# Kernel optimization log

Measured on AMD Instinct MI355X. Metric: run time of the kernel, lower is better.

Reference implementation:

```python
import jax, jax.numpy as jnp
import numpy as np

N, E, B = 50000, 400000, 8
ND, ED, H, L = 32, 16, 128, 3

def setup_inputs() -> dict:
    key = jax.random.key(0)
    ks = jax.random.split(key, 32)
    s = 0.05
    inp = {
        'x': jax.random.normal(ks[0], (N, ND), jnp.float32),
        'edge_attr': jax.random.normal(ks[1], (E, ED), jnp.float32),
        'global_feature': jax.random.normal(ks[2], (B, 1), jnp.float32),
        'edge_index': jax.random.randint(ks[3], (2, E), 0, N, jnp.int64),
        'batch': jnp.sort(jax.random.randint(ks[4], (N,), 0, B, jnp.int64)),
        # embeddings
        'Wn': jax.random.normal(ks[5], (ND, H), jnp.float32) * s,
        'bn': jnp.zeros((H,), jnp.float32),
        'We': jax.random.normal(ks[6], (ED, H), jnp.float32) * s,
        'be': jnp.zeros((H,), jnp.float32),
        'Wg': jax.random.normal(ks[7], (1, H), jnp.float32) * s,
        'bg': jnp.zeros((H,), jnp.float32),
        # message-passing layers (stacked over L)
        'mW1': jax.random.normal(ks[8], (L, 3 * H, H), jnp.float32) * s,
        'mb1': jnp.zeros((L, H), jnp.float32),
        'mW2': jax.random.normal(ks[9], (L, H, H), jnp.float32) * s,
        'mb2': jnp.zeros((L, H), jnp.float32),
        'uW1': jax.random.normal(ks[10], (L, 2 * H, H), jnp.float32) * s,
        'ub1': jnp.zeros((L, H), jnp.float32),
        'uW2': jax.random.normal(ks[11], (L, H, H), jnp.float32) * s,
        'ub2': jnp.zeros((L, H), jnp.float32),
        # readout MLP
        'rW1': jax.random.normal(ks[12], (2 * H, H), jnp.float32) * s,
        'rb1': jnp.zeros((H,), jnp.float32),
        'rW2': jax.random.normal(ks[13], (H, H // 2), jnp.float32) * s,
        'rb2': jnp.zeros((H // 2,), jnp.float32),
        'rW3': jax.random.normal(ks[14], (H // 2, 1), jnp.float32) * s,
        'rb3': jnp.zeros((1,), jnp.float32),
    }
    return inp

def reference(x, edge_attr, global_feature, Wn, bn, We, be, Wg, bg,
              mW1, mb1, mW2, mb2, uW1, ub1, uW2, ub2,
              rW1, rb1, rW2, rb2, rW3, rb3, edge_index, batch):
    h = x @ Wn + bn                      # [N,H]
    e = edge_attr @ We + be              # [E,H]
    g = global_feature @ Wg + bg         # [B,H]
    src, dst = edge_index[0], edge_index[1]  # PyG: x_j=source, x_i=target, aggregate at target
    for l in range(L):
        m_in = jnp.concatenate([h[dst], h[src], e], axis=1)            # [E,3H]
        m = jax.nn.relu(m_in @ mW1[l] + mb1[l]) @ mW2[l] + mb2[l]       # [E,H]
        aggr = jax.ops.segment_sum(m, dst, num_segments=N)              # [N,H]
        u_in = jnp.concatenate([h, aggr], axis=1)                       # [N,2H]
        upd = jax.nn.relu(u_in @ uW1[l] + ub1[l]) @ uW2[l] + ub2[l]
        h = h + upd
    counts = jax.ops.segment_sum(jnp.ones((N,), h.dtype), batch, num_segments=B)
    pooled = jax.ops.segment_sum(h, batch, num_segments=B) / jnp.maximum(counts, 1.0)[:, None]
    final = jnp.concatenate([pooled, g], axis=1)                        # [B,2H]
    out = jax.nn.relu(final @ rW1 + rb1)
    out = jax.nn.relu(out @ rW2 + rb2)
    return out @ rW3 + rb3                                              # [B,1]
```

## Files before the change

kernel.cpp:

```cpp
#include <hip/hip_runtime.h>

#define NN 50000
#define NPAD 50048
#define NBLK 391
#define NE 400000
#define NBATCH 8
#define NDIM 32
#define EDIM 16
#define H 128
#define NLAYERS 3
#define CHUNK_ELEMS 4096
#define NODE_CHUNKS 24
#define ZW_CHUNK 8192
#define NSB 196
#define ZEB 128

typedef __attribute__((ext_vector_type(8))) __bf16 bf16x8;
typedef __attribute__((ext_vector_type(16))) float f32x16;
typedef __attribute__((ext_vector_type(8))) short short8;
typedef __attribute__((ext_vector_type(2))) float v2f;

__device__ __forceinline__ void block_sync_lds() {
  asm volatile("s_waitcnt lgkmcnt(0)\ns_barrier" ::: "memory");
}
__device__ __forceinline__ void wait_lds() {
  asm volatile("s_waitcnt lgkmcnt(0)" ::: "memory");
}
__device__ __forceinline__ v2f bf2f(unsigned u) {
  v2f r;
  r.x = __uint_as_float(u << 16);
  r.y = __uint_as_float(u & 0xffff0000u);
  return r;
}

__global__ __launch_bounds__(128) void embed_nodes_kernel(
    const float* __restrict__ x, const float* __restrict__ Wn,
    const float* __restrict__ bn, __bf16* __restrict__ hb) {
  __shared__ float Ws[NDIM * H];
  __shared__ float xs[16 * NDIM];
  int j = threadIdx.x;
  int nbase = blockIdx.x * 16;
  for (int r = 0; r < NDIM; ++r) Ws[r * H + j] = Wn[r * H + j];
#pragma unroll
  for (int t = 0; t < 4; ++t) {
    int f = j + t * 128;
    xs[f] = x[nbase * NDIM + f];
  }
  __syncthreads();
  float b = bn[j];
  for (int nn = 0; nn < 16; ++nn) {
    float acc = b;
#pragma unroll
    for (int k = 0; k < NDIM; ++k)
      acc = fmaf(xs[nn * NDIM + k], Ws[k * H + j], acc);
    hb[(size_t)(nbase + nn) * H + j] = (__bf16)acc;
  }
}

__global__ __launch_bounds__(256) void degree_kernel(const int* __restrict__ ei,
                                                     int* __restrict__ deg) {
  int e = blockIdx.x * 256 + threadIdx.x;
  if (e < NE) atomicAdd(&deg[ei[NE + e]], 1);
}

__global__ __launch_bounds__(256) void scan1_kernel(const int* __restrict__ deg,
                                                    int* __restrict__ bsum) {
  __shared__ int ws[4];
  int i = blockIdx.x * 256 + threadIdx.x;
  int lane = threadIdx.x & 63, wid = threadIdx.x >> 6;
  int v = (i < NN) ? deg[i] : 0;
#pragma unroll
  for (int off = 32; off; off >>= 1) v += __shfl_down(v, off);
  if (lane == 0) ws[wid] = v;
  __syncthreads();
  if (threadIdx.x == 0) bsum[blockIdx.x] = ws[0] + ws[1] + ws[2] + ws[3];
}

__global__ __launch_bounds__(256) void scan2_kernel(const int* __restrict__ bsum,
                                                    int* __restrict__ boff) {
  __shared__ int s[256];
  int t = threadIdx.x;
  int v = (t < NSB) ? bsum[t] : 0;
  s[t] = v;
  __syncthreads();
  for (int off = 1; off < 256; off <<= 1) {
    int u = (t >= off) ? s[t - off] : 0;
    __syncthreads();
    s[t] += u;
    __syncthreads();
  }
  if (t < NSB) boff[t] = s[t] - v;
}

__global__ __launch_bounds__(256) void scan3_kernel(const int* __restrict__ deg,
                                                    const int* __restrict__ boff,
                                                    int* __restrict__ cursor) {
  __shared__ int wsum[4], woff[4];
  int i = blockIdx.x * 256 + threadIdx.x;
  int lane = threadIdx.x & 63, wid = threadIdx.x >> 6;
  int orig = (i < NN) ? deg[i] : 0;
  int v = orig;
#pragma unroll
  for (int off = 1; off < 64; off <<= 1) {
    int u = __shfl_up(v, off);
    if (lane >= off) v += u;
  }
  if (lane == 63) wsum[wid] = v;
  __syncthreads();
  if (threadIdx.x == 0) {
    int r = 0;
#pragma unroll
    for (int w = 0; w < 4; ++w) {
      woff[w] = r;
      r += wsum[w];
    }
  }
  __syncthreads();
  if (i < NN) cursor[i] = (v - orig) + woff[wid] + boff[blockIdx.x];
}

__global__ __launch_bounds__(256) void scatter_kernel(
    const int* __restrict__ ei, int* __restrict__ cursor,
    int* __restrict__ srcSrt, int* __restrict__ eidSrt) {
  int e = blockIdx.x * 256 + threadIdx.x;
  if (e < NE) {
    int d = ei[NE + e];
    int pos = atomicAdd(&cursor[d], 1);
    srcSrt[pos] = ei[e];
    eidSrt[pos] = e;
  }
}

__global__ __launch_bounds__(256) void gather_ea_kernel(
    const float* __restrict__ ea, const int* __restrict__ eidSrt,
    __bf16* __restrict__ eaSrt) {
  int fl = blockIdx.x * 256 + threadIdx.x;
  if (fl < NE) {
    int e = eidSrt[fl];
    const float4* ep = (const float4*)(ea + (size_t)e * EDIM);
    __bf16* op = eaSrt + (size_t)fl * EDIM;
#pragma unroll
    for (int q = 0; q < 4; ++q) {
      float4 v = ep[q];
      op[q * 4 + 0] = (__bf16)v.x;
      op[q * 4 + 1] = (__bf16)v.y;
      op[q * 4 + 2] = (__bf16)v.z;
      op[q * 4 + 3] = (__bf16)v.w;
    }
  }
}

__global__ __launch_bounds__(256) void precomp_zw_kernel(
    const float* __restrict__ mW1, __bf16* __restrict__ ZW) {
  int l = blockIdx.x / 8;
  int c = blockIdx.x % 8;
  int tid = threadIdx.x;
  const float* w1 = mW1 + (size_t)l * 384 * H;
  __bf16* dst = ZW + ((size_t)l * 8 + c) * ZW_CHUNK;
  for (int it = 0; it < 32; ++it) {
    int flat = it * 256 + tid;
    int j = flat & 7;
    int lane = (flat >> 3) & 63;
    int nt = (flat >> 9) & 7;
    int hilo = flat >> 12;
    int k = c * 16 + ((lane >> 5) << 3) + j;
    int n = nt * 32 + (lane & 31);
    float w = (n < 128) ? w1[(size_t)k * H + n]
                        : w1[(size_t)(128 + k) * H + (n - 128)];
    __bf16 hi = (__bf16)w;
    __bf16 lo = (__bf16)(w - (float)hi);
    dst[flat] = hilo ? lo : hi;
  }
}

__global__ __launch_bounds__(128) void precomp_wef_kernel(
    const float* __restrict__ mW1, const float* __restrict__ mb1,
    const float* __restrict__ We, const float* __restrict__ be,
    float* __restrict__ Wef, float* __restrict__ bm) {
  int l = blockIdx.x;
  int n = threadIdx.x;
  const float* w1 = mW1 + (size_t)l * 384 * H;
  float acc[EDIM];
#pragma unroll
  for (int i = 0; i < EDIM; ++i) acc[i] = 0.f;
  float accb = 0.f;
  for (int c = 0; c < H; ++c) {
    float wv = w1[(size_t)(256 + c) * H + n];
    accb = fmaf(be[c], wv, accb);
#pragma unroll
    for (int i = 0; i < EDIM; ++i)
      acc[i] = fmaf(We[i * H + c], wv, acc[i]);
  }
#pragma unroll
  for (int i = 0; i < EDIM; ++i)
    Wef[((size_t)l * EDIM + i) * H + n] = acc[i];
  bm[l * H + n] = mb1[l * H + n] + accb;
}

__global__ __launch_bounds__(256) void precomp_wefs_kernel(
    const float* __restrict__ Wef, __bf16* __restrict__ WefS) {
  int l = blockIdx.x;
  int tid = threadIdx.x;
  int nt = tid >> 6, lane = tid & 63;
  int n = nt * 32 + (lane & 31);
  int half = lane >> 5;
  const float* wl = Wef + (size_t)l * EDIM * H;
  __bf16* dst = WefS + (size_t)l * CHUNK_ELEMS;
#pragma unroll
  for (int j = 0; j < 8; ++j) {
    int k = half * 8 + j;
    float w = wl[(size_t)k * H + n];
    __bf16 hi = (__bf16)w;
    __bf16 lo = (__bf16)(w - (float)hi);
    dst[((0 * 4 + nt) * 64 + lane) * 8 + j] = hi;
    dst[((1 * 4 + nt) * 64 + lane) * 8 + j] = lo;
  }
}

__global__ __launch_bounds__(128) void precomp_wu_kernel(
    const float* __restrict__ uW1, const float* __restrict__ mW2,
    const float* __restrict__ mb2, float* __restrict__ Wu,
    float* __restrict__ va) {
  int l = blockIdx.x / 257;
  int r = blockIdx.x % 257;
  int j = threadIdx.x;
  const float* u1 = uW1 + (size_t)l * 256 * H;
  if (r < 128) {
    Wu[((size_t)l * 256 + r) * H + j] = u1[(size_t)r * H + j];
  } else if (r < 256) {
    int i = r - 128;
    const float* m2 = mW2 + ((size_t)l * H + i) * H;
    float s = 0.f;
    for (int c = 0; c < H; ++c)
      s = fmaf(m2[c], u1[(size_t)(128 + c) * H + j], s);
    Wu[((size_t)l * 256 + r) * H + j] = s;
  } else {
    float s = 0.f;
    for (int c = 0; c < H; ++c)
      s = fmaf(mb2[l * H + c], u1[(size_t)(128 + c) * H + j], s);
    va[l * H + j] = s;
  }
}

__global__ __launch_bounds__(256) void precomp_wns_kernel(
    const float* __restrict__ Wu, const float* __restrict__ uW2,
    __bf16* __restrict__ WnS) {
  int l = blockIdx.x / NODE_CHUNKS;
  int c = blockIdx.x % NODE_CHUNKS;
  int tid = threadIdx.x;
  int nt = tid >> 6, lane = tid & 63;
  int n = nt * 32 + (lane & 31);
  int half = lane >> 5;
  __bf16* dst = WnS + ((size_t)l * NODE_CHUNKS + c) * CHUNK_ELEMS;
#pragma unroll
  for (int j = 0; j < 8; ++j) {
    float w;
    if (c < 16) {
      int k = c * 16 + half * 8 + j;
      w = Wu[((size_t)l * 256 + k) * H + n];
    } else {
      int k = (c - 16) * 16 + half * 8 + j;
      w = uW2[((size_t)l * H + k) * H + n];
    }
    __bf16 hi = (__bf16)w;
    __bf16 lo = (__bf16)(w - (float)hi);
    dst[((0 * 4 + nt) * 64 + lane) * 8 + j] = hi;
    dst[((1 * 4 + nt) * 64 + lane) * 8 + j] = lo;
  }
}

__global__ __launch_bounds__(256) void zdzs_kernel(
    const __bf16* __restrict__ hb, const __bf16* __restrict__ ZW,
    const float* __restrict__ bm, __bf16* __restrict__ z) {
  __shared__ __align__(16) __bf16 Bt[2][ZW_CHUNK];
  int tid = threadIdx.x;
  int wid = tid >> 6, lane = tid & 63, m = lane & 31, half = lane >> 5;
  int nb = blockIdx.x * 128;
  int row = nb + wid * 32 + m;
  const __bf16* aH = hb + (size_t)row * H + half * 8;
  const short8* gW = (const short8*)ZW;
  short8* sB0 = (short8*)&Bt[0][0];
  short8* sB1 = (short8*)&Bt[1][0];
#pragma unroll
  for (int q = 0; q < 4; ++q) sB0[tid + q * 256] = gW[tid + q * 256];
  short8 p0 = gW[1024 + tid], p1 = gW[1024 + tid + 256];
  short8 p2 = gW[1024 + tid + 512], p3 = gW[1024 + tid + 768];
  f32x16 acc[8];
#pragma unroll
  for (int nt = 0; nt < 8; ++nt)
#pragma unroll
    for (int r = 0; r < 16; ++r) acc[nt][r] = 0.f;
  bf16x8 a = *(const bf16x8*)aH;
  block_sync_lds();

  for (int s = 0; s < 8; ++s) {
    int buf = s & 1;
    bf16x8 na = a;
    if (s + 1 < 8) na = *(const bf16x8*)(aH + (s + 1) * 16);
    if (s + 1 < 8) {
      short8* sb = buf ? sB0 : sB1;
      sb[tid] = p0;
      sb[tid + 256] = p1;
      sb[tid + 512] = p2;
      sb[tid + 768] = p3;
      if (s + 2 < 8) {
        p0 = gW[(size_t)(s + 2) * 1024 + tid];
        p1 = gW[(size_t)(s + 2) * 1024 + tid + 256];
        p2 = gW[(size_t)(s + 2) * 1024 + tid + 512];
        p3 = gW[(size_t)(s + 2) * 1024 + tid + 768];
      }
    }
    const __bf16* bb = &Bt[buf][0];
#pragma unroll
    for (int nt = 0; nt < 8; ++nt) {
      bf16x8 bh = *(const bf16x8*)&bb[((0 * 8 + nt) * 64 + lane) * 8];
      bf16x8 bl = *(const bf16x8*)&bb[((1 * 8 + nt) * 64 + lane) * 8];
      acc[nt] = __builtin_amdgcn_mfma_f32_32x32x16_bf16(a, bh, acc[nt], 0, 0, 0);
      acc[nt] = __builtin_amdgcn_mfma_f32_32x32x16_bf16(a, bl, acc[nt], 0, 0, 0);
    }
    a = na;
    if (s + 1 < 8) block_sync_lds();
  }

  float bmv[4];
#pragma unroll
  for (int nt = 0; nt < 4; ++nt) bmv[nt] = bm[nt * 32 + m];
#pragma unroll
  for (int nt = 0; nt < 8; ++nt) {
    float bias = (nt < 4) ? bmv[nt] : 0.f;
#pragma unroll
    for (int r = 0; r < 16; ++r) {
      int rowi = (r & 3) + 8 * (r >> 2) + 4 * half;
      z[(size_t)(nb + wid * 32 + rowi) * 256 + nt * 32 + m] =
          (__bf16)(acc[nt][r] + bias);
    }
  }
}

__global__ __launch_bounds__(256) void ze_kernel(
    const __bf16* __restrict__ eaSrt, const __bf16* __restrict__ WefS,
    __bf16* __restrict__ zePre) {
  __shared__ __align__(16) __bf16 Bf[CHUNK_ELEMS];
  int tid = threadIdx.x;
  ((short8*)Bf)[tid] = ((const short8*)WefS)[tid];
  ((short8*)Bf)[tid + 256] = ((const short8*)WefS)[tid + 256];
  int wid = tid >> 6, lane = tid & 63, m = lane & 31, half = lane >> 5;
  int ebase = blockIdx.x * ZEB + wid * 32;
  bf16x8 a = *(const bf16x8*)(eaSrt + (size_t)(ebase + m) * EDIM + half * 8);
  f32x16 acc[4];
#pragma unroll
  for (int nt = 0; nt < 4; ++nt)
#pragma unroll
    for (int r = 0; r < 16; ++r) acc[nt][r] = 0.f;
  block_sync_lds();
#pragma unroll
  for (int nt = 0; nt < 4; ++nt) {
    bf16x8 bh = *(const bf16x8*)&Bf[((0 * 4 + nt) * 64 + lane) * 8];
    bf16x8 bl = *(const bf16x8*)&Bf[((1 * 4 + nt) * 64 + lane) * 8];
    acc[nt] = __builtin_amdgcn_mfma_f32_32x32x16_bf16(a, bh, acc[nt], 0, 0, 0);
    acc[nt] = __builtin_amdgcn_mfma_f32_32x32x16_bf16(a, bl, acc[nt], 0, 0, 0);
  }
#pragma unroll
  for (int nt = 0; nt < 4; ++nt) {
#pragma unroll
    for (int r = 0; r < 16; ++r) {
      int rowi = (r & 3) + 8 * (r >> 2) + 4 * half;
      zePre[(size_t)(ebase + rowi) * H + nt * 32 + m] = (__bf16)acc[nt][r];
    }
  }
}

__global__ __launch_bounds__(256) void edge_aggr_kernel(
    const __bf16* __restrict__ z, const int* __restrict__ srcSrt,
    const int* __restrict__ cend, const __bf16* __restrict__ zePre,
    float* __restrict__ aggrH) {
  int node = blockIdx.x * 4 + (threadIdx.x >> 6);
  int lane = threadIdx.x & 63;
  int c0 = lane * 2;
  int end = cend[node];
  int start = node ? cend[node - 1] : 0;
  v2f acc = {0.f, 0.f};
  if (start < end) {
    v2f zd = bf2f(*(const unsigned*)(z + (size_t)node * 256 + c0));
    int sArr[4];
#pragma unroll
    for (int p = 0; p < 4; ++p)
      if (start + p < end) sArr[p] = srcSrt[start + p];
    for (int e0 = start; e0 < end; e0 += 4) {
      unsigned zsb[4], zeb[4];
#pragma unroll
      for (int p = 0; p < 4; ++p) {
        if (e0 + p < end) {
          zsb[p] = *(const unsigned*)(z + (size_t)sArr[p] * 256 + 128 + c0);
          zeb[p] = *(const unsigned*)(zePre + (size_t)(e0 + p) * H + c0);
        }
      }
#pragma unroll
      for (int p = 0; p < 4; ++p)
        if (e0 + 4 + p < end) sArr[p] = srcSrt[e0 + 4 + p];
#pragma unroll
      for (int p = 0; p < 4; ++p) {
        if (e0 + p < end) {
          v2f t = zd + bf2f(zsb[p]) + bf2f(zeb[p]);
          acc.x += fmaxf(t.x, 0.f);
          acc.y += fmaxf(t.y, 0.f);
        }
      }
    }
  }
  *(v2f*)(aggrH + (size_t)node * H + c0) = acc;
}

__global__ __launch_bounds__(256) void node_update_mfma_kernel(
    __bf16* __restrict__ hb, const float* __restrict__ aggrH,
    const int* __restrict__ deg, const __bf16* __restrict__ WnS,
    const float* __restrict__ ub1, const float* __restrict__ va,
    const float* __restrict__ ub2) {
  __shared__ __align__(16) __bf16 Bt[2][CHUNK_ELEMS];
  __shared__ __bf16 hid[4][32][132];
  __shared__ float degS[128];
  int tid = threadIdx.x;
  int nb = blockIdx.x * 128;
  if (tid < 128) degS[tid] = (float)deg[nb + tid];
  int wid = tid >> 6, lane = tid & 63, m = lane & 31, half = lane >> 5;
  int row = nb + wid * 32 + m;
  const __bf16* aHb = hb + (size_t)row * H + half * 8;
  const float* aG = aggrH + (size_t)row * H + half * 8;
  const short8* gW = (const short8*)WnS;
  short8* sB0 = (short8*)&Bt[0][0];
  short8* sB1 = (short8*)&Bt[1][0];
  sB0[tid] = gW[tid];
  sB0[tid + 256] = gW[tid + 256];
  short8 p0 = gW[512 + tid], p1 = gW[512 + tid + 256];
  float bv1[4], bva[4];
#pragma unroll
  for (int nt = 0; nt < 4; ++nt) {
    bv1[nt] = ub1[nt * 32 + m];
    bva[nt] = va[nt * 32 + m];
  }
  f32x16 acc[4];
#pragma unroll
  for (int nt = 0; nt < 4; ++nt)
#pragma unroll
    for (int r = 0; r < 16; ++r) acc[nt][r] = 0.f;
  bf16x8 acur = *(const bf16x8*)aHb;
  block_sync_lds();

  for (int s = 0; s < 16; ++s) {
    int buf = s & 1;
    bf16x8 anext = acur;
    if (s + 1 < 16) {
      int sp = s + 1;
      if (sp < 8) {
        anext = *(const bf16x8*)(aHb + sp * 16);
      } else {
        const float* pp = aG + (sp - 8) * 16;
        float4 f0 = *(const float4*)pp;
        float4 f1 = *(const float4*)(pp + 4);
        float af[8] = {f0.x, f0.y, f0.z, f0.w, f1.x, f1.y, f1.z, f1.w};
#pragma unroll
        for (int j = 0; j < 8; ++j) anext[j] = (__bf16)af[j];
      }
    }
    {
      short8* sb = buf ? sB0 : sB1;
      sb[tid] = p0;
      sb[tid + 256] = p1;
      if (s + 2 < NODE_CHUNKS) {
        p0 = gW[(size_t)(s + 2) * 512 + tid];
        p1 = gW[(size_t)(s + 2) * 512 + tid + 256];
      }
    }
    const __bf16* bb = &Bt[buf][0];
#pragma unroll
    for (int nt = 0; nt < 4; ++nt) {
      bf16x8 bh = *(const bf16x8*)&bb[((0 * 4 + nt) * 64 + lane) * 8];
      bf16x8 bl = *(const bf16x8*)&bb[((1 * 4 + nt) * 64 + lane) * 8];
      acc[nt] = __builtin_amdgcn_mfma_f32_32x32x16_bf16(acur, bh, acc[nt], 0, 0, 0);
      acc[nt] = __builtin_amdgcn_mfma_f32_32x32x16_bf16(acur, bl, acc[nt], 0, 0, 0);
    }
    acur = anext;
    block_sync_lds();
  }

#pragma unroll
  for (int nt = 0; nt < 4; ++nt) {
#pragma unroll
    for (int r = 0; r < 16; ++r) {
      int rowi = (r & 3) + 8 * (r >> 2) + 4 * half;
      float v = acc[nt][r] + bv1[nt] + degS[wid * 32 + rowi] * bva[nt];
      hid[wid][rowi][nt * 32 + m] = (__bf16)fmaxf(v, 0.f);
      acc[nt][r] = 0.f;
    }
  }
  wait_lds();

  for (int s = 16; s < NODE_CHUNKS; ++s) {
    int buf = s & 1;
    if (s + 1 < NODE_CHUNKS) {
      short8* sb = buf ? sB0 : sB1;
      sb[tid] = p0;
      sb[tid + 256] = p1;
      if (s + 2 < NODE_CHUNKS) {
        p0 = gW[(size_t)(s + 2) * 512 + tid];
        p1 = gW[(size_t)(s + 2) * 512 + tid + 256];
      }
    }
    bf16x8 ah = *(const bf16x8*)&hid[wid][m][(s - 16) * 16 + half * 8];
    const __bf16* bb = &Bt[buf][0];
#pragma unroll
    for (int nt = 0; nt < 4; ++nt) {
      bf16x8 bh = *(const bf16x8*)&bb[((0 * 4 + nt) * 64 + lane) * 8];
      bf16x8 bl = *(const bf16x8*)&bb[((1 * 4 + nt) * 64 + lane) * 8];
      acc[nt] = __builtin_amdgcn_mfma_f32_32x32x16_bf16(ah, bh, acc[nt], 0, 0, 0);
      acc[nt] = __builtin_amdgcn_mfma_f32_32x32x16_bf16(ah, bl, acc[nt], 0, 0, 0);
    }
    if (s + 1 < NODE_CHUNKS) block_sync_lds();
  }

#pragma unroll
  for (int nt = 0; nt < 4; ++nt) {
    float b2 = ub2[nt * 32 + m];
#pragma unroll
    for (int r = 0; r < 16; ++r) {
      int rowi = (r & 3) + 8 * (r >> 2) + 4 * half;
      size_t idx = (size_t)(nb + wid * 32 + rowi) * H + nt * 32 + m;
      float hv = (float)hb[idx];
      hb[idx] = (__bf16)(hv + acc[nt][r] + b2);
    }
  }
}

__global__ __launch_bounds__(128) void pool_kernel(
    const __bf16* __restrict__ hb, const int* __restrict__ batch,
    float* __restrict__ pooled, int* __restrict__ counts) {
  int j = threadIdx.x;
  int nbase = blockIdx.x * 128;
  int nend = nbase + 128;
  if (nend > NN) nend = NN;
  if (nbase >= NN) return;
  int cur = batch[nbase];
  float sum = 0.f;
  int cnt = 0;
  for (int n = nbase; n < nend; ++n) {
    int b = batch[n];
    if (b != cur) {
      unsafeAtomicAdd(&pooled[cur * H + j], sum);
      if (j == 0) atomicAdd(&counts[cur], cnt);
      sum = 0.f; cnt = 0; cur = b;
    }
    sum += (float)hb[(size_t)n * H + j];
    cnt++;
  }
  unsafeAtomicAdd(&pooled[cur * H + j], sum);
  if (j == 0) atomicAdd(&counts[cur], cnt);
}

__global__ __launch_bounds__(128) void readout_kernel(
    const float* __restrict__ pooled, const int* __restrict__ counts,
    const float* __restrict__ gf, const float* __restrict__ Wg,
    const float* __restrict__ bg, const float* __restrict__ rW1,
    const float* __restrict__ rb1, const float* __restrict__ rW2,
    const float* __restrict__ rb2, const float* __restrict__ rW3,
    const float* __restrict__ rb3, float* __restrict__ out) {
  __shared__ float fin[256];
  __shared__ float t1[128];
  __shared__ float t2[64];
  int j = threadIdx.x;
  int b = blockIdx.x;
  float cnt = (float)counts[b];
  if (cnt < 1.f) cnt = 1.f;
  fin[j] = pooled[b * H + j] / cnt;
  fin[H + j] = fmaf(gf[b], Wg[j], bg[j]);
  __syncthreads();
  float a = rb1[j];
  for (int k = 0; k < 256; ++k) a = fmaf(fin[k], rW1[k * H + j], a);
  t1[j] = fmaxf(a, 0.f);
  __syncthreads();
  if (j < 64) {
    float a2 = rb2[j];
    for (int k = 0; k < 128; ++k) a2 = fmaf(t1[k], rW2[k * 64 + j], a2);
    t2[j] = fmaxf(a2, 0.f);
  }
  __syncthreads();
  if (j < 64) {
    float p = t2[j] * rW3[j];
#pragma unroll
    for (int off = 32; off; off >>= 1) p += __shfl_down(p, off);
    if (j == 0) out[b] = p + rb3[0];
  }
}

extern "C" void kernel_launch(void* const* d_in, const int* in_sizes, int n_in,
                              void* d_out, int out_size, void* d_ws, size_t ws_size,
                              hipStream_t stream) {
  const float* x   = (const float*)d_in[0];
  const float* ea  = (const float*)d_in[1];
  const float* gf  = (const float*)d_in[2];
  const int*   ei  = (const int*)d_in[3];
  const int*   bat = (const int*)d_in[4];
  const float* Wn  = (const float*)d_in[5];
  const float* bn  = (const float*)d_in[6];
  const float* We  = (const float*)d_in[7];
  const float* be  = (const float*)d_in[8];
  const float* Wg  = (const float*)d_in[9];
  const float* bg  = (const float*)d_in[10];
  const float* mW1 = (const float*)d_in[11];
  const float* mb1 = (const float*)d_in[12];
  const float* mW2 = (const float*)d_in[13];
  const float* mb2 = (const float*)d_in[14];
  const float* uW1 = (const float*)d_in[15];
  const float* ub1 = (const float*)d_in[16];
  const float* uW2 = (const float*)d_in[17];
  const float* ub2 = (const float*)d_in[18];
  const float* rW1 = (const float*)d_in[19];
  const float* rb1 = (const float*)d_in[20];
  const float* rW2 = (const float*)d_in[21];
  const float* rb2 = (const float*)d_in[22];
  const float* rW3 = (const float*)d_in[23];
  const float* rb3 = (const float*)d_in[24];

  char* p = (char*)d_ws;
  __bf16* hb     = (__bf16*)p; p += (size_t)NPAD * H * 2;
  float*  aggrH  = (float*)p;  p += (size_t)NPAD * H * 4;
  __bf16* z      = (__bf16*)p; p += (size_t)NPAD * 256 * 2;
  __bf16* zePre  = (__bf16*)p; p += (size_t)NE * H * 2;
  __bf16* eaSrt  = (__bf16*)p; p += (size_t)NE * EDIM * 2;
  int*    srcSrt = (int*)p;    p += (size_t)NE * 4;
  int*    eidSrt = (int*)p;    p += (size_t)NE * 4;
  __bf16* ZW     = (__bf16*)p; p += (size_t)NLAYERS * 8 * ZW_CHUNK * 2;
  __bf16* WnS    = (__bf16*)p; p += (size_t)NLAYERS * NODE_CHUNKS * CHUNK_ELEMS * 2;
  __bf16* WefS   = (__bf16*)p; p += (size_t)NLAYERS * CHUNK_ELEMS * 2;
  float*  Wef    = (float*)p;  p += (size_t)NLAYERS * EDIM * H * 4;
  float*  bm     = (float*)p;  p += (size_t)NLAYERS * H * 4;
  float*  Wu     = (float*)p;  p += (size_t)NLAYERS * 256 * H * 4;
  float*  va     = (float*)p;  p += (size_t)NLAYERS * H * 4;
  int*    deg    = (int*)p;    p += (size_t)NPAD * 4;
  int*    cursor = (int*)p;    p += (size_t)NPAD * 4;
  int*    bsum   = (int*)p;    p += 256 * 4;
  int*    boff   = (int*)p;    p += 256 * 4;
  float*  pooled = (float*)p;  p += (size_t)NBATCH * H * 4;
  int*    counts = (int*)p;    p += 64;

  hipMemsetAsync(deg, 0, (size_t)NPAD * 4, stream);
  hipMemsetAsync(cursor, 0, (size_t)NPAD * 4, stream);
  hipMemsetAsync(pooled, 0, (size_t)NBATCH * H * 4, stream);
  hipMemsetAsync(counts, 0, 64, stream);

  embed_nodes_kernel<<<NN / 16, 128, 0, stream>>>(x, Wn, bn, hb);
  degree_kernel<<<(NE + 255) / 256, 256, 0, stream>>>(ei, deg);
  scan1_kernel<<<NSB, 256, 0, stream>>>(deg, bsum);
  scan2_kernel<<<1, 256, 0, stream>>>(bsum, boff);
  scan3_kernel<<<NSB, 256, 0, stream>>>(deg, boff, cursor);
  scatter_kernel<<<(NE + 255) / 256, 256, 0, stream>>>(ei, cursor, srcSrt, eidSrt);
  gather_ea_kernel<<<(NE + 255) / 256, 256, 0, stream>>>(ea, eidSrt, eaSrt);
  precomp_zw_kernel<<<NLAYERS * 8, 256, 0, stream>>>(mW1, ZW);
  precomp_wef_kernel<<<NLAYERS, 128, 0, stream>>>(mW1, mb1, We, be, Wef, bm);
  precomp_wefs_kernel<<<NLAYERS, 256, 0, stream>>>(Wef, WefS);
  precomp_wu_kernel<<<NLAYERS * 257, 128, 0, stream>>>(uW1, mW2, mb2, Wu, va);
  precomp_wns_kernel<<<NLAYERS * NODE_CHUNKS, 256, 0, stream>>>(Wu, uW2, WnS);

  for (int l = 0; l < NLAYERS; ++l) {
    zdzs_kernel<<<NBLK, 256, 0, stream>>>(
        hb, ZW + (size_t)l * 8 * ZW_CHUNK, bm + (size_t)l * H, z);
    ze_kernel<<<NE / ZEB, 256, 0, stream>>>(
        eaSrt, WefS + (size_t)l * CHUNK_ELEMS, zePre);
    edge_aggr_kernel<<<NPAD / 4, 256, 0, stream>>>(
        z, srcSrt, cursor, zePre, aggrH);
    node_update_mfma_kernel<<<NBLK, 256, 0, stream>>>(
        hb, aggrH, deg, WnS + (size_t)l * NODE_CHUNKS * CHUNK_ELEMS,
        ub1 + (size_t)l * H, va + (size_t)l * H, ub2 + (size_t)l * H);
  }

  pool_kernel<<<(NN + 127) / 128, 128, 0, stream>>>(hb, bat, pooled, counts);
  readout_kernel<<<NBATCH, 128, 0, stream>>>(pooled, counts, gf, Wg, bg, rW1,
                                             rb1, rW2, rb2, rW3, rb3,
                                             (float*)d_out);
}
```

Measured before the change: 571.6 us.

## Split node-update tiles across warps by column and vectorize pooling with LDS atomics

The node update kernel now processes 64 rows per block instead of 128. Each pair of warps shares a 32-row group and each warp computes half of the output columns, which doubles the grid to raise occupancy and parallelism. Because the hidden tile is now shared between warps, a block-wide barrier replaces the per-warp wait. The pool kernel is rewritten to use 256 threads with vectorized bf16 loads and per-block LDS atomics, flushing to global once per block, which cuts serial per-node loops and global atomic traffic. The cost is redundant A-operand loads across warp pairs and extra barriers.

```diff
diff --git a/kernel.cpp b/kernel.cpp
--- a/kernel.cpp
+++ b/kernel.cpp
@@ -417,13 +417,15 @@
     const float* __restrict__ ub1, const float* __restrict__ va,
     const float* __restrict__ ub2) {
   __shared__ __align__(16) __bf16 Bt[2][CHUNK_ELEMS];
-  __shared__ __bf16 hid[4][32][132];
-  __shared__ float degS[128];
+  __shared__ __bf16 hid[2][32][132];
+  __shared__ float degS[64];
   int tid = threadIdx.x;
-  int nb = blockIdx.x * 128;
-  if (tid < 128) degS[tid] = (float)deg[nb + tid];
+  int nb = blockIdx.x * 64;
+  if (tid < 64) degS[tid] = (float)deg[nb + tid];
   int wid = tid >> 6, lane = tid & 63, m = lane & 31, half = lane >> 5;
-  int row = nb + wid * 32 + m;
+  int rg = wid & 1;
+  int nh = wid >> 1;
+  int row = nb + rg * 32 + m;
   const __bf16* aHb = hb + (size_t)row * H + half * 8;
   const float* aG = aggrH + (size_t)row * H + half * 8;
   const short8* gW = (const short8*)WnS;
@@ -432,17 +434,18 @@
   sB0[tid] = gW[tid];
   sB0[tid + 256] = gW[tid + 256];
   short8 p0 = gW[512 + tid], p1 = gW[512 + tid + 256];
-  float bv1[4], bva[4];
-#pragma unroll
-  for (int nt = 0; nt < 4; ++nt) {
-    bv1[nt] = ub1[nt * 32 + m];
-    bva[nt] = va[nt * 32 + m];
-  }
-  f32x16 acc[4];
-#pragma unroll
-  for (int nt = 0; nt < 4; ++nt)
-#pragma unroll
-    for (int r = 0; r < 16; ++r) acc[nt][r] = 0.f;
+  float bv1[2], bva[2];
+#pragma unroll
+  for (int ntl = 0; ntl < 2; ++ntl) {
+    int nt = nh * 2 + ntl;
+    bv1[ntl] = ub1[nt * 32 + m];
+    bva[ntl] = va[nt * 32 + m];
+  }
+  f32x16 acc[2];
+#pragma unroll
+  for (int ntl = 0; ntl < 2; ++ntl)
+#pragma unroll
+    for (int r = 0; r < 16; ++r) acc[ntl][r] = 0.f;
   bf16x8 acur = *(const bf16x8*)aHb;
   block_sync_lds();
 
@@ -473,27 +476,29 @@
     }
     const __bf16* bb = &Bt[buf][0];
 #pragma unroll
-    for (int nt = 0; nt < 4; ++nt) {
+    for (int ntl = 0; ntl < 2; ++ntl) {
+      int nt = nh * 2 + ntl;
       bf16x8 bh = *(const bf16x8*)&bb[((0 * 4 + nt) * 64 + lane) * 8];
       bf16x8 bl = *(const bf16x8*)&bb[((1 * 4 + nt) * 64 + lane) * 8];
-      acc[nt] = __builtin_amdgcn_mfma_f32_32x32x16_bf16(acur, bh, acc[nt], 0, 0, 0);
-      acc[nt] = __builtin_amdgcn_mfma_f32_32x32x16_bf16(acur, bl, acc[nt], 0, 0, 0);
+      acc[ntl] = __builtin_amdgcn_mfma_f32_32x32x16_bf16(acur, bh, acc[ntl], 0, 0, 0);
+      acc[ntl] = __builtin_amdgcn_mfma_f32_32x32x16_bf16(acur, bl, acc[ntl], 0, 0, 0);
     }
     acur = anext;
     block_sync_lds();
   }
 
 #pragma unroll
-  for (int nt = 0; nt < 4; ++nt) {
+  for (int ntl = 0; ntl < 2; ++ntl) {
+    int nt = nh * 2 + ntl;
 #pragma unroll
     for (int r = 0; r < 16; ++r) {
       int rowi = (r & 3) + 8 * (r >> 2) + 4 * half;
-      float v = acc[nt][r] + bv1[nt] + degS[wid * 32 + rowi] * bva[nt];
-      hid[wid][rowi][nt * 32 + m] = (__bf16)fmaxf(v, 0.f);
-      acc[nt][r] = 0.f;
-    }
-  }
-  wait_lds();
+      float v = acc[ntl][r] + bv1[ntl] + degS[rg * 32 + rowi] * bva[ntl];
+      hid[rg][rowi][nt * 32 + m] = (__bf16)fmaxf(v, 0.f);
+      acc[ntl][r] = 0.f;
+    }
+  }
+  block_sync_lds();
 
   for (int s = 16; s < NODE_CHUNKS; ++s) {
     int buf = s & 1;
@@ -506,54 +511,91 @@
         p1 = gW[(size_t)(s + 2) * 512 + tid + 256];
       }
     }
-    bf16x8 ah = *(const bf16x8*)&hid[wid][m][(s - 16) * 16 + half * 8];
+    bf16x8 ah = *(const bf16x8*)&hid[rg][m][(s - 16) * 16 + half * 8];
     const __bf16* bb = &Bt[buf][0];
 #pragma unroll
-    for (int nt = 0; nt < 4; ++nt) {
+    for (int ntl = 0; ntl < 2; ++ntl) {
+      int nt = nh * 2 + ntl;
       bf16x8 bh = *(const bf16x8*)&bb[((0 * 4 + nt) * 64 + lane) * 8];
       bf16x8 bl = *(const bf16x8*)&bb[((1 * 4 + nt) * 64 + lane) * 8];
-      acc[nt] = __builtin_amdgcn_mfma_f32_32x32x16_bf16(ah, bh, acc[nt], 0, 0, 0);
-      acc[nt] = __builtin_amdgcn_mfma_f32_32x32x16_bf16(ah, bl, acc[nt], 0, 0, 0);
+      acc[ntl] = __builtin_amdgcn_mfma_f32_32x32x16_bf16(ah, bh, acc[ntl], 0, 0, 0);
+      acc[ntl] = __builtin_amdgcn_mfma_f32_32x32x16_bf16(ah, bl, acc[ntl], 0, 0, 0);
     }
     if (s + 1 < NODE_CHUNKS) block_sync_lds();
   }
 
 #pragma unroll
-  for (int nt = 0; nt < 4; ++nt) {
+  for (int ntl = 0; ntl < 2; ++ntl) {
+    int nt = nh * 2 + ntl;
     float b2 = ub2[nt * 32 + m];
 #pragma unroll
     for (int r = 0; r < 16; ++r) {
       int rowi = (r & 3) + 8 * (r >> 2) + 4 * half;
-      size_t idx = (size_t)(nb + wid * 32 + rowi) * H + nt * 32 + m;
+      size_t idx = (size_t)(nb + rg * 32 + rowi) * H + nt * 32 + m;
       float hv = (float)hb[idx];
-      hb[idx] = (__bf16)(hv + acc[nt][r] + b2);
-    }
-  }
-}
-
-__global__ __launch_bounds__(128) void pool_kernel(
+      hb[idx] = (__bf16)(hv + acc[ntl][r] + b2);
+    }
+  }
+}
+
+__global__ __launch_bounds__(256) void pool_kernel(
     const __bf16* __restrict__ hb, const int* __restrict__ batch,
     float* __restrict__ pooled, int* __restrict__ counts) {
-  int j = threadIdx.x;
+  __shared__ float pS[NBATCH * H];
+  __shared__ int cS[NBATCH];
+  int tid = threadIdx.x;
+  for (int i = tid; i < NBATCH * H; i += 256) pS[i] = 0.f;
+  if (tid < NBATCH) cS[tid] = 0;
+  __syncthreads();
+  int c = tid & 15;
+  int r0 = tid >> 4;
   int nbase = blockIdx.x * 128;
-  int nend = nbase + 128;
-  if (nend > NN) nend = NN;
-  if (nbase >= NN) return;
-  int cur = batch[nbase];
-  float sum = 0.f;
+  v2f acc4[4] = {{0.f, 0.f}, {0.f, 0.f}, {0.f, 0.f}, {0.f, 0.f}};
   int cnt = 0;
-  for (int n = nbase; n < nend; ++n) {
+  int cur = -1;
+#pragma unroll
+  for (int i = 0; i < 8; ++i) {
+    int n = nbase + i * 16 + r0;
+    if (n >= NN) break;
     int b = batch[n];
     if (b != cur) {
-      unsafeAtomicAdd(&pooled[cur * H + j], sum);
-      if (j == 0) atomicAdd(&counts[cur], cnt);
-      sum = 0.f; cnt = 0; cur = b;
-    }
-    sum += (float)hb[(size_t)n * H + j];
+      if (cur >= 0) {
+#pragma unroll
+        for (int q = 0; q < 4; ++q) {
+          atomicAdd(&pS[cur * H + c * 8 + q * 2], acc4[q].x);
+          atomicAdd(&pS[cur * H + c * 8 + q * 2 + 1], acc4[q].y);
+          acc4[q].x = 0.f;
+          acc4[q].y = 0.f;
+        }
+        if (c == 0) atomicAdd(&cS[cur], cnt);
+        cnt = 0;
+      }
+      cur = b;
+    }
+    uint4 v = *(const uint4*)(hb + (size_t)n * H + c * 8);
+    acc4[0] += bf2f(v.x);
+    acc4[1] += bf2f(v.y);
+    acc4[2] += bf2f(v.z);
+    acc4[3] += bf2f(v.w);
     cnt++;
   }
-  unsafeAtomicAdd(&pooled[cur * H + j], sum);
-  if (j == 0) atomicAdd(&counts[cur], cnt);
+  if (cur >= 0) {
+#pragma unroll
+    for (int q = 0; q < 4; ++q) {
+      atomicAdd(&pS[cur * H + c * 8 + q * 2], acc4[q].x);
+      atomicAdd(&pS[cur * H + c * 8 + q * 2 + 1], acc4[q].y);
+    }
+    if (c == 0) atomicAdd(&cS[cur], cnt);
+  }
+  __syncthreads();
+  for (int i = tid; i < NBATCH * H; i += 256) {
+    float v = pS[i];
+    if (v != 0.f) unsafeAtomicAdd(&pooled[i], v);
+  }
+  if (tid < NBATCH) {
+    int cv = cS[tid];
+    if (cv) atomicAdd(&counts[tid], cv);
+  }
 }
 
 __global__ __launch_bounds__(128) void readout_kernel(
@@ -667,12 +709,12 @@
         eaSrt, WefS + (size_t)l * CHUNK_ELEMS, zePre);
     edge_aggr_kernel<<<NPAD / 4, 256, 0, stream>>>(
         z, srcSrt, cursor, zePre, aggrH);
-    node_update_mfma_kernel<<<NBLK, 256, 0, stream>>>(
+    node_update_mfma_kernel<<<NPAD / 64, 256, 0, stream>>>(
         hb, aggrH, deg, WnS + (size_t)l * NODE_CHUNKS * CHUNK_ELEMS,
         ub1 + (size_t)l * H, va + (size_t)l * H, ub2 + (size_t)l * H);
   }
 
-  pool_kernel<<<(NN + 127) / 128, 128, 0, stream>>>(hb, bat, pooled, counts);
+  pool_kernel<<<NPAD / 128, 256, 0, stream>>>(hb, bat, pooled, counts);
   readout_kernel<<<NBATCH, 128, 0, stream>>>(pooled, counts, gf, Wg, bg, rW1,
                                              rb1, rW2, rb2, rW3, rb3,
                                              (float*)d_out);
```

New measurement: 563.8 us. About the same (-1.4%).
